# Kernel optimization log

Hardware: AMD Instinct MI355X
Metric: run time of the kernel (lower is better)

Reference implementation:

```python
import jax, jax.numpy as jnp
import numpy as np

TOP_K = 9  # ATSSMatcher default


def setup_inputs() -> dict:
    key = jax.random.key(0)
    k1, k2, k3, k4 = jax.random.split(key, 4)
    N, M = 120000, 800
    IMG = 1024.0
    # anchors: valid x1<x2, y1<y2 boxes
    a_ctr = jax.random.uniform(k1, (N, 2)) * IMG
    a_sz = jax.random.uniform(k2, (N, 2)) * 60.0 + 8.0
    anchors = jnp.concatenate([a_ctr - a_sz / 2, a_ctr + a_sz / 2], axis=1)
    g_ctr = jax.random.uniform(k3, (M, 2)) * IMG
    g_sz = jax.random.uniform(k4, (M, 2)) * 100.0 + 10.0
    gt_boxes = jnp.concatenate([g_ctr - g_sz / 2, g_ctr + g_sz / 2], axis=1)
    return {"anchors": anchors, "gt_boxes": gt_boxes}


def _box_iou(a, b):
    # a: [N,4], b: [M,4] -> [N,M]
    area_a = (a[:, 2] - a[:, 0]) * (a[:, 3] - a[:, 1])
    area_b = (b[:, 2] - b[:, 0]) * (b[:, 3] - b[:, 1])
    lt = jnp.maximum(a[:, None, :2], b[None, :, :2])
    rb = jnp.minimum(a[:, None, 2:], b[None, :, 2:])
    wh = jnp.clip(rb - lt, 0.0)
    inter = wh[..., 0] * wh[..., 1]
    union = area_a[:, None] + area_b[None, :] - inter
    return inter / jnp.maximum(union, 1e-12)


def reference(anchors, gt_boxes):
    N = anchors.shape[0]
    M = gt_boxes.shape[0]
    ious = _box_iou(anchors, gt_boxes)                         # [N, M]
    a_ctr = (anchors[:, :2] + anchors[:, 2:]) / 2              # [N, 2]
    g_ctr = (gt_boxes[:, :2] + gt_boxes[:, 2:]) / 2            # [M, 2]
    # center distances [M, N] (per-GT rows for top-k along last axis)
    d = jnp.linalg.norm(a_ctr[None, :, :] - g_ctr[:, None, :], axis=-1)
    _, topk_idx = jax.lax.top_k(-d, TOP_K)                     # [M, TOP_K] nearest anchors
    topk_ious = jnp.take_along_axis(ious.T, topk_idx, axis=1)  # [M, TOP_K]
    iou_mean = topk_ious.mean(axis=1)                          # [M]
    iou_std = jnp.std(topk_ious, axis=1, ddof=1)               # torch .std() is unbiased
    thresh = iou_mean + iou_std                                # [M]
    candidate = ious >= thresh[None, :]                        # [N, M]
    cx, cy = a_ctr[:, 0], a_ctr[:, 1]
    inside = ((cx[:, None] >= gt_boxes[None, :, 0]) &
              (cx[:, None] <= gt_boxes[None, :, 2]) &
              (cy[:, None] >= gt_boxes[None, :, 1]) &
              (cy[:, None] <= gt_boxes[None, :, 3]))           # [N, M]
    pos = candidate & inside                                   # [N, M]
    gt_ids = jnp.arange(M, dtype=jnp.int32)[None, :]
    matched_idxs = jnp.max(jnp.where(pos, gt_ids, -1), axis=1)  # [N]
    gathered = jnp.take_along_axis(
        ious, jnp.clip(matched_idxs, 0)[:, None].astype(jnp.int32), axis=1)[:, 0]
    max_ious = jnp.where(matched_idxs >= 0, gathered, 0.0)
    return matched_idxs.astype(jnp.int64), max_ious
```

## Files before the change

kernel.cpp:

```cpp
#include <hip/hip_runtime.h>
#include <stdint.h>

typedef unsigned int u32;
typedef unsigned long long u64;

#define TOPK 9
#define GA 64
#define CELL_A 16.0f
#define NCA (GA * GA)
#define GG 16
#define CELL_G 64.0f
#define NCG (GG * GG)
#define CAPA 96
#define CAPG 160
#define OVA 8192
#define OVG 1024

__global__ __launch_bounds__(256) void zero_counts(u32* __restrict__ p, int n)
{
    int i = blockIdx.x * 256 + threadIdx.x;
    if (i < n) p[i] = 0u;
}

__global__ __launch_bounds__(256) void bucket_insert(
    const float4* __restrict__ a4, const float4* __restrict__ g4,
    u32* __restrict__ cursA, u32* __restrict__ cursG, u32* __restrict__ ovfCnt,
    float4* __restrict__ slotA, float4* __restrict__ gtBox,
    u32* __restrict__ gtBkt,
    u32* __restrict__ ovAidx, float2* __restrict__ ovActr,
    u32* __restrict__ ovGidx, int N, int M)
{
    int gid = blockIdx.x * 256 + threadIdx.x;
    if (gid < N) {
        float4 a = a4[gid];
        float cx = (a.x + a.z) * 0.5f;
        float cy = (a.y + a.w) * 0.5f;
        int ix = min(GA - 1, max(0, (int)(cx * (1.0f / CELL_A))));
        int iy = min(GA - 1, max(0, (int)(cy * (1.0f / CELL_A))));
        int cell = iy * GA + ix;
        u32 p = atomicAdd(&cursA[cell], 1u);
        if (p < CAPA) {
            slotA[cell * CAPA + p] =
                make_float4(cx, cy, __uint_as_float((u32)gid), 0.f);
        } else {
            u32 q = atomicAdd(&ovfCnt[0], 1u);
            if (q < OVA) { ovAidx[q] = (u32)gid; ovActr[q] = make_float2(cx, cy); }
        }
    } else if (gid < N + M) {
        int m = gid - N;
        float4 g = g4[m];
        int ix0 = min(GG - 1, max(0, (int)floorf(g.x * (1.0f / CELL_G))));
        int iy0 = min(GG - 1, max(0, (int)floorf(g.y * (1.0f / CELL_G))));
        int ix1 = min(GG - 1, max(0, (int)floorf(g.z * (1.0f / CELL_G))));
        int iy1 = min(GG - 1, max(0, (int)floorf(g.w * (1.0f / CELL_G))));
        for (int j = iy0; j <= iy1; ++j)
            for (int i = ix0; i <= ix1; ++i) {
                int cell = j * GG + i;
                u32 p = atomicAdd(&cursG[cell], 1u);
                if (p < CAPG) {
                    gtBox[cell * CAPG + p] = g;
                    gtBkt[cell * CAPG + p] = (u32)m;
                } else {
                    u32 q = atomicAdd(&ovfCnt[1], 1u);
                    if (q < OVG) ovGidx[q] = (u32)m;
                }
            }
    }
}

__global__ __launch_bounds__(256) void atss_query(
    const float4* __restrict__ a4, const float* __restrict__ gts,
    const u32* __restrict__ cursA, const float4* __restrict__ slotA,
    const u32* __restrict__ ovfCnt,
    const u32* __restrict__ ovAidx, const float2* __restrict__ ovActr,
    float* __restrict__ thresh, int M)
{
    const int m = blockIdx.x;
    if (m >= M) return;
    const int tid  = (int)threadIdx.x;
    const int wid  = tid >> 6;
    const int lane = tid & 63;

    __shared__ u32   s_cnt[4];
    __shared__ float s_max[4];
    __shared__ u64   s_top[4 * TOPK];

    const float gx0 = gts[m * 4 + 0], gy0 = gts[m * 4 + 1];
    const float gx1 = gts[m * 4 + 2], gy1 = gts[m * 4 + 3];
    const float gcx = (gx0 + gx1) * 0.5f;
    const float gcy = (gy0 + gy1) * 0.5f;
    const int ci = min(GA - 1, max(0, (int)(gcx * (1.0f / CELL_A))));
    const int cj = min(GA - 1, max(0, (int)(gcy * (1.0f / CELL_A))));

    {
        const int r = wid;
        const int ncell = (r == 0) ? 1 : 8 * r;
        u32 myc = 0;
        float mymax = 0.f;
        for (int k = lane; k < ncell; k += 64) {
            int di = 0, dj = 0;
            if (r > 0) {
                int side = k / (2 * r), pos = k % (2 * r);
                if (side == 0)      { di = -r + pos; dj = -r; }
                else if (side == 1) { di = r;        dj = -r + pos; }
                else if (side == 2) { di = r - pos;  dj = r; }
                else                { di = -r;       dj = r - pos; }
            }
            int i = ci + di, j = cj + dj;
            if (i < 0 || i >= GA || j < 0 || j >= GA) continue;
            u32 cnt = cursA[j * GA + i];
            if (cnt) {
                myc += cnt;
                float x0 = i * CELL_A, x1 = x0 + CELL_A;
                float y0 = j * CELL_A, y1 = y0 + CELL_A;
                float dxm = fmaxf(gcx - x0, x1 - gcx);
                float dym = fmaxf(gcy - y0, y1 - gcy);
                mymax = fmaxf(mymax, dxm * dxm + dym * dym);
            }
        }
#pragma unroll
        for (int s2 = 1; s2 <= 32; s2 <<= 1) {
            myc += __shfl_xor(myc, s2, 64);
            mymax = fmaxf(mymax, __shfl_xor(mymax, s2, 64));
        }
        if (lane == 0) { s_cnt[wid] = myc; s_max[wid] = mymax; }
    }
    __syncthreads();

    u32 cum = 0;
    float maxd2 = 0.f;
#pragma unroll
    for (int r = 0; r < 4; ++r) {
        if (cum < TOPK) {
            cum += s_cnt[r];
            maxd2 = fmaxf(maxd2, s_max[r]);
        }
    }
    if (cum < TOPK) {
        for (int r = 4; r < GA && cum < TOPK; ++r) {
            const int ncell = 8 * r;
            u32 myc = 0;
            float mymax = 0.f;
            for (int k = lane; k < ncell; k += 64) {
                int side = k / (2 * r), pos = k % (2 * r);
                int di, dj;
                if (side == 0)      { di = -r + pos; dj = -r; }
                else if (side == 1) { di = r;        dj = -r + pos; }
                else if (side == 2) { di = r - pos;  dj = r; }
                else                { di = -r;       dj = r - pos; }
                int i = ci + di, j = cj + dj;
                if (i < 0 || i >= GA || j < 0 || j >= GA) continue;
                u32 cnt = cursA[j * GA + i];
                if (cnt) {
                    myc += cnt;
                    float x0 = i * CELL_A, x1 = x0 + CELL_A;
                    float y0 = j * CELL_A, y1 = y0 + CELL_A;
                    float dxm = fmaxf(gcx - x0, x1 - gcx);
                    float dym = fmaxf(gcy - y0, y1 - gcy);
                    mymax = fmaxf(mymax, dxm * dxm + dym * dym);
                }
            }
#pragma unroll
            for (int s2 = 1; s2 <= 32; s2 <<= 1) {
                myc += __shfl_xor(myc, s2, 64);
                mymax = fmaxf(mymax, __shfl_xor(mymax, s2, 64));
            }
            cum += myc;
            maxd2 = fmaxf(maxd2, mymax);
        }
    }
    const float D2pad = maxd2 * 1.0001f + 1.0f;

    u64 kk[TOPK];
#pragma unroll
    for (int i = 0; i < TOPK; ++i) kk[i] = ~0ULL;

    const int rs = 1 + (int)(sqrtf(D2pad) * (1.0f / CELL_A));
    const int jlo = max(0, cj - rs), jhi = min(GA - 1, cj + rs);
    const int ilo = max(0, ci - rs), ihi = min(GA - 1, ci + rs);
    const int ncols  = ihi - ilo + 1;
    const int ncells = (jhi - jlo + 1) * ncols;
    for (int t = wid; t < ncells; t += 4) {
        int j = jlo + t / ncols;
        int i = ilo + t % ncols;
        float y0 = j * CELL_A, y1 = y0 + CELL_A;
        float mdy = fmaxf(fmaxf(y0 - gcy, gcy - y1), 0.f);
        float x0 = i * CELL_A, x1 = x0 + CELL_A;
        float mdx = fmaxf(fmaxf(x0 - gcx, gcx - x1), 0.f);
        if (mdx * mdx + mdy * mdy > D2pad) continue;
        int c = j * GA + i;
        u32 cnt = min(cursA[c], (u32)CAPA);
        u32 base = (u32)c * CAPA;
        for (u32 tc = lane; tc < cnt; tc += 64) {
            float4 s = slotA[base + tc];
            float ddx = s.x - gcx, ddy = s.y - gcy;
            float d2 = ddx * ddx + ddy * ddy;
            if (d2 <= D2pad) {
                float d = sqrtf(d2);
                u64 key = ((u64)__float_as_uint(d) << 32) | __float_as_uint(s.z);
                if (key < kk[TOPK - 1]) {
                    u64 t2 = key;
#pragma unroll
                    for (int q = 0; q < TOPK; ++q) {
                        u64 lo = (kk[q] < t2) ? kk[q] : t2;
                        u64 hi = (kk[q] < t2) ? t2 : kk[q];
                        kk[q] = lo;
                        t2 = hi;
                    }
                }
            }
        }
    }
    {
        u32 nov = min(ovfCnt[0], (u32)OVA);
        for (u32 tc = (u32)tid; tc < nov; tc += 256) {
            u32 n = ovAidx[tc];
            float2 cc = ovActr[tc];
            float ddx = cc.x - gcx, ddy = cc.y - gcy;
            float d2 = ddx * ddx + ddy * ddy;
            if (d2 <= D2pad) {
                float d = sqrtf(d2);
                u64 key = ((u64)__float_as_uint(d) << 32) | n;
                if (key < kk[TOPK - 1]) {
                    u64 t2 = key;
#pragma unroll
                    for (int q = 0; q < TOPK; ++q) {
                        u64 lo = (kk[q] < t2) ? kk[q] : t2;
                        u64 hi = (kk[q] < t2) ? t2 : kk[q];
                        kk[q] = lo;
                        t2 = hi;
                    }
                }
            }
        }
    }

    {
        u64 wv;
#pragma unroll
        for (int rd = 0; rd < TOPK; ++rd) {
            wv = kk[0];
#pragma unroll
            for (int s2 = 1; s2 <= 32; s2 <<= 1) {
                u64 o = __shfl_xor(wv, s2, 64);
                if (o < wv) wv = o;
            }
            if (lane == 0) s_top[wid * TOPK + rd] = wv;
            if (kk[0] == wv) {
#pragma unroll
                for (int q = 0; q < TOPK - 1; ++q) kk[q] = kk[q + 1];
                kk[TOPK - 1] = ~0ULL;
            }
        }
    }
    __syncthreads();

    if (wid == 0) {
        u64 v = (lane < 4 * TOPK) ? s_top[lane] : ~0ULL;
        u64 wins[TOPK];
#pragma unroll
        for (int rd = 0; rd < TOPK; ++rd) {
            u64 wv = v;
#pragma unroll
            for (int s2 = 1; s2 <= 32; s2 <<= 1) {
                u64 o = __shfl_xor(wv, s2, 64);
                if (o < wv) wv = o;
            }
            wins[rd] = wv;
            if (v == wv) v = ~0ULL;
        }

        if (lane == 0) {
            const float area_g = (gx1 - gx0) * (gy1 - gy0);
            float vals[TOPK];
            float sum = 0.f;
#pragma unroll
            for (int r = 0; r < TOPK; ++r) {
                int idx = (int)(u32)(wins[r] & 0xffffffffULL);
                float4 a = a4[idx];
                float area_a = (a.z - a.x) * (a.w - a.y);
                float ltx = fmaxf(a.x, gx0), lty = fmaxf(a.y, gy0);
                float rbx = fminf(a.z, gx1), rby = fminf(a.w, gy1);
                float w2 = fmaxf(rbx - ltx, 0.f);
                float h2 = fmaxf(rby - lty, 0.f);
                float inter = w2 * h2;
                float uni = area_a + area_g - inter;
                float iou = inter / fmaxf(uni, 1e-12f);
                vals[r] = iou;
                sum += iou;
            }
            float mean = sum / 9.0f;
            float var = 0.f;
#pragma unroll
            for (int r = 0; r < TOPK; ++r) {
                float d2 = vals[r] - mean;
                var += d2 * d2;
            }
            float sd = sqrtf(var / 8.0f);
            thresh[m] = mean + sd;
        }
    }
}

__global__ __launch_bounds__(256) void atss_assign(
    const float4* __restrict__ a4, const float4* __restrict__ g4,
    const float* __restrict__ thresh,
    const u32* __restrict__ cursG, const float4* __restrict__ gtBox,
    const u32* __restrict__ gtBkt,
    const u32* __restrict__ ovfCnt, const u32* __restrict__ ovGidx,
    float* __restrict__ out_idx, float* __restrict__ out_iou, int N, int M)
{
    int n = blockIdx.x * 256 + threadIdx.x;
    if (n >= N) return;

    float4 a = a4[n];
    float area_a = (a.z - a.x) * (a.w - a.y);
    float cx = (a.x + a.z) * 0.5f;
    float cy = (a.y + a.w) * 0.5f;

    int ig = min(GG - 1, max(0, (int)(cx * (1.0f / CELL_G))));
    int jg = min(GG - 1, max(0, (int)(cy * (1.0f / CELL_G))));
    int cell = jg * GG + ig;

    u64 best = 0;
    u32 cnt = min(cursG[cell], (u32)CAPG);
    u32 base = (u32)cell * CAPG;
    for (u32 t2 = 0; t2 < cnt; ++t2) {
        float4 g = gtBox[base + t2];
        if (cx >= g.x && cx <= g.z && cy >= g.y && cy <= g.w) {
            int mi = (int)gtBkt[base + t2];
            float area_g = (g.z - g.x) * (g.w - g.y);
            float ltx = fmaxf(a.x, g.x), lty = fmaxf(a.y, g.y);
            float rbx = fminf(a.z, g.z), rby = fminf(a.w, g.w);
            float w = fmaxf(rbx - ltx, 0.f);
            float h = fmaxf(rby - lty, 0.f);
            float inter = w * h;
            float uni = area_a + area_g - inter;
            float iou = inter / fmaxf(uni, 1e-12f);
            if (iou >= thresh[mi]) {
                u64 cand = ((u64)(u32)(mi + 1) << 32) | __float_as_uint(iou);
                if (cand > best) best = cand;
            }
        }
    }
    {
        u32 nog = min(ovfCnt[1], (u32)OVG);
        for (u32 t2 = 0; t2 < nog; ++t2) {
            int mi = (int)ovGidx[t2];
            float4 g = g4[mi];
            if (cx >= g.x && cx <= g.z && cy >= g.y && cy <= g.w) {
                float area_g = (g.z - g.x) * (g.w - g.y);
                float ltx = fmaxf(a.x, g.x), lty = fmaxf(a.y, g.y);
                float rbx = fminf(a.z, g.z), rby = fminf(a.w, g.w);
                float w = fmaxf(rbx - ltx, 0.f);
                float h = fmaxf(rby - lty, 0.f);
                float inter = w * h;
                float uni = area_a + area_g - inter;
                float iou = inter / fmaxf(uni, 1e-12f);
                if (iou >= thresh[mi]) {
                    u64 cand = ((u64)(u32)(mi + 1) << 32) | __float_as_uint(iou);
                    if (cand > best) best = cand;
                }
            }
        }
    }

    int mm = (int)(best >> 32) - 1;
    out_idx[n] = (float)mm;
    out_iou[n] = (mm >= 0) ? __uint_as_float((u32)best) : 0.f;
}

__global__ __launch_bounds__(256) void fb_centers(
    const float4* __restrict__ a4, float2* __restrict__ c2, int N)
{
    int n = blockIdx.x * 256 + threadIdx.x;
    if (n < N) {
        float4 a = a4[n];
        c2[n] = make_float2((a.x + a.z) * 0.5f, (a.y + a.w) * 0.5f);
    }
}

__global__ __launch_bounds__(256) void fb_thresh(
    const float4* __restrict__ a4, const float2* __restrict__ c2,
    const float* __restrict__ gts, float* __restrict__ thresh, int N)
{
    const int m = blockIdx.x;
    const int tid = threadIdx.x;
    const float gx0 = gts[m * 4 + 0], gy0 = gts[m * 4 + 1];
    const float gx1 = gts[m * 4 + 2], gy1 = gts[m * 4 + 3];
    const float gcx = (gx0 + gx1) * 0.5f;
    const float gcy = (gy0 + gy1) * 0.5f;

    float vmin = __builtin_inff();
    for (int n = tid; n < N; n += 512) {
        float2 c = c2[n];
        float dx = c.x - gcx, dy = c.y - gcy;
        vmin = fminf(vmin, dx * dx + dy * dy);
    }
    float v = vmin, w = 0.f;
#pragma unroll
    for (int r = 0; r < TOPK; ++r) {
        float t = v;
#pragma unroll
        for (int s = 1; s <= 32; s <<= 1) t = fminf(t, __shfl_xor(t, s, 64));
        w = t;
        if (v == w) v = __builtin_inff();
    }
    const float T = sqrtf(w) * 1.0001f + 1e-6f;

    u64 k[TOPK];
#pragma unroll
    for (int i = 0; i < TOPK; ++i) k[i] = ~0ULL;
    for (int n = tid; n < N; n += 256) {
        float2 c = c2[n];
        float dx = c.x - gcx, dy = c.y - gcy;
        float d = sqrtf(dx * dx + dy * dy);
        if (d <= T) {
            u64 key = ((u64)__float_as_uint(d) << 32) | (unsigned)n;
            if (key < k[TOPK - 1]) {
                u64 t = key;
#pragma unroll
                for (int i = 0; i < TOPK; ++i) {
                    u64 lo = (k[i] < t) ? k[i] : t;
                    u64 hi = (k[i] < t) ? t : k[i];
                    k[i] = lo;
                    t = hi;
                }
            }
        }
    }
    __shared__ u64 red[256];
    __shared__ int top9[TOPK];
#pragma unroll 1
    for (int r = 0; r < TOPK; ++r) {
        red[tid] = k[0];
        __syncthreads();
        for (int s = 128; s > 0; s >>= 1) {
            if (tid < s) {
                u64 o = red[tid + s];
                if (o < red[tid]) red[tid] = o;
            }
            __syncthreads();
        }
        u64 win = red[0];
        if (tid == 0) top9[r] = (int)(unsigned)(win & 0xffffffffULL);
        __syncthreads();
        if (k[0] == win) {
#pragma unroll
            for (int i = 0; i < TOPK - 1; ++i) k[i] = k[i + 1];
            k[TOPK - 1] = ~0ULL;
        }
    }
    if (tid == 0) {
        const float area_g = (gx1 - gx0) * (gy1 - gy0);
        float vals[TOPK];
        float s = 0.f;
#pragma unroll
        for (int r = 0; r < TOPK; ++r) {
            float4 a = a4[top9[r]];
            float area_a = (a.z - a.x) * (a.w - a.y);
            float ltx = fmaxf(a.x, gx0), lty = fmaxf(a.y, gy0);
            float rbx = fminf(a.z, gx1), rby = fminf(a.w, gy1);
            float w2 = fmaxf(rbx - ltx, 0.f);
            float h2 = fmaxf(rby - lty, 0.f);
            float inter = w2 * h2;
            float uni = area_a + area_g - inter;
            float iou = inter / fmaxf(uni, 1e-12f);
            vals[r] = iou;
            s += iou;
        }
        float mean = s / 9.0f;
        float var = 0.f;
#pragma unroll
        for (int r = 0; r < TOPK; ++r) {
            float d2 = vals[r] - mean;
            var += d2 * d2;
        }
        thresh[m] = mean + sqrtf(var / 8.0f);
    }
}

__global__ __launch_bounds__(256) void fb_assign(
    const float4* __restrict__ a4, const float4* __restrict__ g4,
    const float* __restrict__ thresh,
    float* __restrict__ out_idx, float* __restrict__ out_iou, int N, int M)
{
    extern __shared__ char smem[];
    float4* sg = (float4*)smem;
    float2* se = (float2*)(smem + (size_t)M * 16);
    for (int i = threadIdx.x; i < M; i += 256) {
        float4 g = g4[i];
        sg[i] = g;
        se[i] = make_float2((g.z - g.x) * (g.w - g.y), thresh[i]);
    }
    __syncthreads();
    int n = blockIdx.x * 256 + threadIdx.x;
    if (n >= N) return;
    float4 a = a4[n];
    float area_a = (a.z - a.x) * (a.w - a.y);
    float cx = (a.x + a.z) * 0.5f;
    float cy = (a.y + a.w) * 0.5f;
    u64 best = 0;
    for (int mi = 0; mi < M; ++mi) {
        float4 g = sg[mi];
        if (cx >= g.x && cx <= g.z && cy >= g.y && cy <= g.w) {
            float2 e = se[mi];
            float ltx = fmaxf(a.x, g.x), lty = fmaxf(a.y, g.y);
            float rbx = fminf(a.z, g.z), rby = fminf(a.w, g.w);
            float w = fmaxf(rbx - ltx, 0.f);
            float h = fmaxf(rby - lty, 0.f);
            float inter = w * h;
            float uni = area_a + e.x - inter;
            float iou = inter / fmaxf(uni, 1e-12f);
            if (iou >= e.y)
                best = ((u64)(u32)(mi + 1) << 32) | __float_as_uint(iou);
        }
    }
    int mm = (int)(best >> 32) - 1;
    out_idx[n] = (float)mm;
    out_iou[n] = (mm >= 0) ? __uint_as_float((u32)best) : 0.f;
}

extern "C" void kernel_launch(void* const* d_in, const int* in_sizes, int n_in,
                              void* d_out, int out_size, void* d_ws, size_t ws_size,
                              hipStream_t stream) {
    const float4* a4 = (const float4*)d_in[0];
    const float4* g4 = (const float4*)d_in[1];
    const float* gts = (const float*)d_in[1];
    const int N = in_sizes[0] / 4;
    const int M = in_sizes[1] / 4;

    const size_t oCursA  = 0;
    const size_t oCursG  = oCursA + NCA;
    const size_t oOvfCnt = oCursG + NCG;
    const size_t oThresh = oOvfCnt + 2;
    size_t oSlotA = oThresh + (size_t)M;
    oSlotA = (oSlotA + 3) & ~(size_t)3;
    const size_t oGtBox  = oSlotA + 4 * (size_t)NCA * CAPA;
    const size_t oGtBkt  = oGtBox + 4 * (size_t)NCG * CAPG;
    const size_t oOvAidx = oGtBkt + (size_t)NCG * CAPG;
    size_t oOvActr = oOvAidx + OVA;
    oOvActr = (oOvActr + 1) & ~(size_t)1;
    const size_t oOvGidx = oOvActr + 2 * (size_t)OVA;
    const size_t needBytes = (oOvGidx + OVG) * sizeof(u32);

    if (ws_size >= needBytes) {
        u32* w = (u32*)d_ws;
        u32* cursA    = w + oCursA;
        u32* cursG    = w + oCursG;
        u32* ovfCnt   = w + oOvfCnt;
        float* thr    = (float*)(w + oThresh);
        float4* slotA = (float4*)(w + oSlotA);
        float4* gtBox = (float4*)(w + oGtBox);
        u32* gtBkt    = w + oGtBkt;
        u32* ovAidx   = w + oOvAidx;
        float2* ovActr= (float2*)(w + oOvActr);
        u32* ovGidx   = w + oOvGidx;

        const int nZero = NCA + NCG + 2;
        zero_counts<<<(nZero + 255) / 256, 256, 0, stream>>>(cursA, nZero);
        bucket_insert<<<(N + M + 255) / 256, 256, 0, stream>>>(
            a4, g4, cursA, cursG, ovfCnt, slotA, gtBox, gtBkt,
            ovAidx, ovActr, ovGidx, N, M);
        atss_query<<<M, 256, 0, stream>>>(
            a4, gts, cursA, slotA, ovfCnt, ovAidx, ovActr, thr, M);
        atss_assign<<<(N + 255) / 256, 256, 0, stream>>>(
            a4, g4, thr, cursG, gtBox, gtBkt, ovfCnt, ovGidx,
            (float*)d_out, (float*)d_out + N, N, M);
    } else {
        float* thr = (float*)d_ws;
        float2* centers = (float2*)d_out;
        fb_centers<<<(N + 255) / 256, 256, 0, stream>>>(a4, centers, N);
        fb_thresh<<<M, 256, 0, stream>>>(a4, (const float2*)centers, gts, thr, N);
        size_t lds = (size_t)M * 24;
        fb_assign<<<(N + 255) / 256, 256, lds, stream>>>(
            a4, g4, thr, (float*)d_out, (float*)d_out + N, N, M);
    }
}
```

Before: 49.71 us.

## Fuse four launches into two cooperative kernels with in-kernel grid synchronisation

```diff
diff --git a/kernel.cpp b/kernel.cpp
--- a/kernel.cpp
+++ b/kernel.cpp
@@ -15,6 +15,446 @@
 #define CAPG 160
 #define OVA 8192
 #define OVG 1024
+
+#define MAGA 0x5A17C3D9u
+#define MAGB 0xA6E83C26u
+
+__device__ __forceinline__ u32 aload(const u32* p) {
+    return __hip_atomic_load(p, __ATOMIC_RELAXED, __HIP_MEMORY_SCOPE_AGENT);
+}
+__device__ __forceinline__ void astore(u32* p, u32 v) {
+    __hip_atomic_store(p, v, __ATOMIC_RELAXED, __HIP_MEMORY_SCOPE_AGENT);
+}
+
+#define ZN (NCA + NCG + 2 + 1)
+
+__global__ __launch_bounds__(256) void insert_init(
+    const float4* __restrict__ a4, const float4* __restrict__ g4,
+    u32* __restrict__ w, int N, int M)
+{
+    const size_t oCursA  = 0;
+    const size_t oCursG  = oCursA + NCA;
+    const size_t oOvfCnt = oCursG + NCG;
+    const size_t oQdone  = oOvfCnt + 2;
+    const size_t oMag    = oQdone + 1;
+    size_t oThresh = oMag + 2;
+    size_t oSlotA  = (oThresh + (size_t)M + 3) & ~(size_t)3;
+    const size_t oGtBox  = oSlotA + 4 * (size_t)NCA * CAPA;
+    const size_t oGtBkt  = oGtBox + 4 * (size_t)NCG * CAPG;
+    const size_t oOvAidx = oGtBkt + (size_t)NCG * CAPG;
+    size_t oOvActr = (oOvAidx + OVA + 1) & ~(size_t)1;
+    const size_t oOvGidx = oOvActr + 2 * (size_t)OVA;
+
+    u32* cursA    = w + oCursA;
+    u32* cursG    = w + oCursG;
+    u32* ovfCnt   = w + oOvfCnt;
+    u32* mag      = w + oMag;
+    float4* slotA = (float4*)(w + oSlotA);
+    float4* gtBox = (float4*)(w + oGtBox);
+    u32* gtBkt    = w + oGtBkt;
+    u32* ovAidx   = w + oOvAidx;
+    float2* ovActr= (float2*)(w + oOvActr);
+    u32* ovGidx   = w + oOvGidx;
+
+    const int tid = (int)threadIdx.x;
+    const int bid = (int)blockIdx.x;
+
+    if (bid == 0) {
+        for (int i = tid; i < ZN; i += 256) astore(&w[i], 0u);
+        asm volatile("s_waitcnt vmcnt(0)" ::: "memory");
+        __syncthreads();
+        if (tid == 0) { astore(&mag[0], MAGA); astore(&mag[1], MAGB); }
+    } else {
+        if (tid == 0) {
+            while (!(aload(&mag[0]) == MAGA && aload(&mag[1]) == MAGB))
+                __builtin_amdgcn_s_sleep(4);
+        }
+        __syncthreads();
+    }
+
+    const int gstride = (int)gridDim.x * 256;
+    for (int gid = bid * 256 + tid; gid < N + M; gid += gstride) {
+        if (gid < N) {
+            float4 a = a4[gid];
+            float cx = (a.x + a.z) * 0.5f;
+            float cy = (a.y + a.w) * 0.5f;
+            int ix = min(GA - 1, max(0, (int)(cx * (1.0f / CELL_A))));
+            int iy = min(GA - 1, max(0, (int)(cy * (1.0f / CELL_A))));
+            int cell = iy * GA + ix;
+            u32 p = atomicAdd(&cursA[cell], 1u);
+            if (p < CAPA) {
+                slotA[cell * CAPA + p] =
+                    make_float4(cx, cy, __uint_as_float((u32)gid), 0.f);
+            } else {
+                u32 q = atomicAdd(&ovfCnt[0], 1u);
+                if (q < OVA) { ovAidx[q] = (u32)gid; ovActr[q] = make_float2(cx, cy); }
+            }
+        } else {
+            int m = gid - N;
+            float4 g = g4[m];
+            int ix0 = min(GG - 1, max(0, (int)floorf(g.x * (1.0f / CELL_G))));
+            int iy0 = min(GG - 1, max(0, (int)floorf(g.y * (1.0f / CELL_G))));
+            int ix1 = min(GG - 1, max(0, (int)floorf(g.z * (1.0f / CELL_G))));
+            int iy1 = min(GG - 1, max(0, (int)floorf(g.w * (1.0f / CELL_G))));
+            for (int j = iy0; j <= iy1; ++j)
+                for (int i = ix0; i <= ix1; ++i) {
+                    int cell = j * GG + i;
+                    u32 p = atomicAdd(&cursG[cell], 1u);
+                    if (p < CAPG) {
+                        gtBox[cell * CAPG + p] = g;
+                        gtBkt[cell * CAPG + p] = (u32)m;
+                    } else {
+                        u32 q = atomicAdd(&ovfCnt[1], 1u);
+                        if (q < OVG) ovGidx[q] = (u32)m;
+                    }
+                }
+        }
+    }
+}
+
+__global__ __launch_bounds__(256) void qa_fused(
+    const float4* __restrict__ a4, const float4* __restrict__ g4,
+    u32* __restrict__ w, float* __restrict__ outp, int N, int M)
+{
+    const size_t oCursA  = 0;
+    const size_t oCursG  = oCursA + NCA;
+    const size_t oOvfCnt = oCursG + NCG;
+    const size_t oQdone  = oOvfCnt + 2;
+    const size_t oMag    = oQdone + 1;
+    size_t oThresh = oMag + 2;
+    size_t oSlotA  = (oThresh + (size_t)M + 3) & ~(size_t)3;
+    const size_t oGtBox  = oSlotA + 4 * (size_t)NCA * CAPA;
+    const size_t oGtBkt  = oGtBox + 4 * (size_t)NCG * CAPG;
+    const size_t oOvAidx = oGtBkt + (size_t)NCG * CAPG;
+    size_t oOvActr = (oOvAidx + OVA + 1) & ~(size_t)1;
+    const size_t oOvGidx = oOvActr + 2 * (size_t)OVA;
+
+    const u32* cursA    = w + oCursA;
+    const u32* cursG    = w + oCursG;
+    const u32* ovfCnt   = w + oOvfCnt;
+    u32* qdone          = w + oQdone;
+    u32* mag            = w + oMag;
+    u32* thr            = w + oThresh;
+    const float4* slotA = (const float4*)(w + oSlotA);
+    const float4* gtBox = (const float4*)(w + oGtBox);
+    const u32* gtBkt    = w + oGtBkt;
+    const u32* ovAidx   = w + oOvAidx;
+    const float2* ovActr= (const float2*)(w + oOvActr);
+    const u32* ovGidx   = w + oOvGidx;
+    const float* gts = (const float*)g4;
+    float* out_idx = outp;
+    float* out_iou = outp + N;
+
+    const int tid  = (int)threadIdx.x;
+    const int bid  = (int)blockIdx.x;
+    const int nblk = (int)gridDim.x;
+    const int wid  = tid >> 6;
+    const int lane = tid & 63;
+
+    __shared__ u32   s_cnt[4];
+    __shared__ float s_max[4];
+    __shared__ u64   s_top[4 * TOPK];
+    __shared__ float s_thr[2048];
+
+    for (int m = bid; m < M; m += nblk) {
+        const float gx0 = gts[m * 4 + 0], gy0 = gts[m * 4 + 1];
+        const float gx1 = gts[m * 4 + 2], gy1 = gts[m * 4 + 3];
+        const float gcx = (gx0 + gx1) * 0.5f;
+        const float gcy = (gy0 + gy1) * 0.5f;
+        const int ci = min(GA - 1, max(0, (int)(gcx * (1.0f / CELL_A))));
+        const int cj = min(GA - 1, max(0, (int)(gcy * (1.0f / CELL_A))));
+
+        {
+            const int r = wid;
+            const int ncell = (r == 0) ? 1 : 8 * r;
+            u32 myc = 0;
+            float mymax = 0.f;
+            for (int k = lane; k < ncell; k += 64) {
+                int di = 0, dj = 0;
+                if (r > 0) {
+                    int side = k / (2 * r), pos = k % (2 * r);
+                    if (side == 0)      { di = -r + pos; dj = -r; }
+                    else if (side == 1) { di = r;        dj = -r + pos; }
+                    else if (side == 2) { di = r - pos;  dj = r; }
+                    else                { di = -r;       dj = r - pos; }
+                }
+                int i = ci + di, j = cj + dj;
+                if (i < 0 || i >= GA || j < 0 || j >= GA) continue;
+                u32 cnt = cursA[j * GA + i];
+                if (cnt) {
+                    myc += cnt;
+                    float x0 = i * CELL_A, x1 = x0 + CELL_A;
+                    float y0 = j * CELL_A, y1 = y0 + CELL_A;
+                    float dxm = fmaxf(gcx - x0, x1 - gcx);
+                    float dym = fmaxf(gcy - y0, y1 - gcy);
+                    mymax = fmaxf(mymax, dxm * dxm + dym * dym);
+                }
+            }
+#pragma unroll
+            for (int s2 = 1; s2 <= 32; s2 <<= 1) {
+                myc += __shfl_xor(myc, s2, 64);
+                mymax = fmaxf(mymax, __shfl_xor(mymax, s2, 64));
+            }
+            if (lane == 0) { s_cnt[wid] = myc; s_max[wid] = mymax; }
+        }
+        __syncthreads();
+
+        u32 cum = 0;
+        float maxd2 = 0.f;
+#pragma unroll
+        for (int r = 0; r < 4; ++r) {
+            if (cum < TOPK) {
+                cum += s_cnt[r];
+                maxd2 = fmaxf(maxd2, s_max[r]);
+            }
+        }
+        __syncthreads();
+        if (cum < TOPK) {
+            for (int r = 4; r < GA && cum < TOPK; ++r) {
+                const int ncell = 8 * r;
+                u32 myc = 0;
+                float mymax = 0.f;
+                for (int k = lane; k < ncell; k += 64) {
+                    int side = k / (2 * r), pos = k % (2 * r);
+                    int di, dj;
+                    if (side == 0)      { di = -r + pos; dj = -r; }
+                    else if (side == 1) { di = r;        dj = -r + pos; }
+                    else if (side == 2) { di = r - pos;  dj = r; }
+                    else                { di = -r;       dj = r - pos; }
+                    int i = ci + di, j = cj + dj;
+                    if (i < 0 || i >= GA || j < 0 || j >= GA) continue;
+                    u32 cnt = cursA[j * GA + i];
+                    if (cnt) {
+                        myc += cnt;
+                        float x0 = i * CELL_A, x1 = x0 + CELL_A;
+                        float y0 = j * CELL_A, y1 = y0 + CELL_A;
+                        float dxm = fmaxf(gcx - x0, x1 - gcx);
+                        float dym = fmaxf(gcy - y0, y1 - gcy);
+                        mymax = fmaxf(mymax, dxm * dxm + dym * dym);
+                    }
+                }
+#pragma unroll
+                for (int s2 = 1; s2 <= 32; s2 <<= 1) {
+                    myc += __shfl_xor(myc, s2, 64);
+                    mymax = fmaxf(mymax, __shfl_xor(mymax, s2, 64));
+                }
+                cum += myc;
+                maxd2 = fmaxf(maxd2, mymax);
+            }
+        }
+        const float D2pad = maxd2 * 1.0001f + 1.0f;
+
+        u64 kk[TOPK];
+#pragma unroll
+        for (int i = 0; i < TOPK; ++i) kk[i] = ~0ULL;
+
+        const int rs = 1 + (int)(sqrtf(D2pad) * (1.0f / CELL_A));
+        const int jlo = max(0, cj - rs), jhi = min(GA - 1, cj + rs);
+        const int ilo = max(0, ci - rs), ihi = min(GA - 1, ci + rs);
+        const int ncols  = ihi - ilo + 1;
+        const int ncells = (jhi - jlo + 1) * ncols;
+        for (int t = wid; t < ncells; t += 4) {
+            int j = jlo + t / ncols;
+            int i = ilo + t % ncols;
+            float y0 = j * CELL_A, y1 = y0 + CELL_A;
+            float mdy = fmaxf(fmaxf(y0 - gcy, gcy - y1), 0.f);
+            float x0 = i * CELL_A, x1 = x0 + CELL_A;
+            float mdx = fmaxf(fmaxf(x0 - gcx, gcx - x1), 0.f);
+            if (mdx * mdx + mdy * mdy > D2pad) continue;
+            int c = j * GA + i;
+            u32 cnt = min(cursA[c], (u32)CAPA);
+            u32 base = (u32)c * CAPA;
+            for (u32 tc = lane; tc < cnt; tc += 64) {
+                float4 s = slotA[base + tc];
+                float ddx = s.x - gcx, ddy = s.y - gcy;
+                float d2 = ddx * ddx + ddy * ddy;
+                if (d2 <= D2pad) {
+                    float d = sqrtf(d2);
+                    u64 key = ((u64)__float_as_uint(d) << 32) | __float_as_uint(s.z);
+                    if (key < kk[TOPK - 1]) {
+                        u64 t2 = key;
+#pragma unroll
+                        for (int q = 0; q < TOPK; ++q) {
+                            u64 lo = (kk[q] < t2) ? kk[q] : t2;
+                            u64 hi = (kk[q] < t2) ? t2 : kk[q];
+                            kk[q] = lo;
+                            t2 = hi;
+                        }
+                    }
+                }
+            }
+        }
+        {
+            u32 nov = min(ovfCnt[0], (u32)OVA);
+            for (u32 tc = (u32)tid; tc < nov; tc += 256) {
+                u32 n = ovAidx[tc];
+                float2 cc = ovActr[tc];
+                float ddx = cc.x - gcx, ddy = cc.y - gcy;
+                float d2 = ddx * ddx + ddy * ddy;
+                if (d2 <= D2pad) {
+                    float d = sqrtf(d2);
+                    u64 key = ((u64)__float_as_uint(d) << 32) | n;
+                    if (key < kk[TOPK - 1]) {
+                        u64 t2 = key;
+#pragma unroll
+                        for (int q = 0; q < TOPK; ++q) {
+                            u64 lo = (kk[q] < t2) ? kk[q] : t2;
+                            u64 hi = (kk[q] < t2) ? t2 : kk[q];
+                            kk[q] = lo;
+                            t2 = hi;
+                        }
+                    }
+                }
+            }
+        }
+
+        {
+#pragma unroll
+            for (int rd = 0; rd < TOPK; ++rd) {
+                u64 wv = kk[0];
+#pragma unroll
+                for (int s2 = 1; s2 <= 32; s2 <<= 1) {
+                    u64 o = __shfl_xor(wv, s2, 64);
+                    if (o < wv) wv = o;
+                }
+                if (lane == 0) s_top[wid * TOPK + rd] = wv;
+                if (kk[0] == wv) {
+#pragma unroll
+                    for (int q = 0; q < TOPK - 1; ++q) kk[q] = kk[q + 1];
+                    kk[TOPK - 1] = ~0ULL;
+                }
+            }
+        }
+        __syncthreads();
+
+        if (wid == 0) {
+            u64 v = (lane < 4 * TOPK) ? s_top[lane] : ~0ULL;
+            u64 wins[TOPK];
+#pragma unroll
+            for (int rd = 0; rd < TOPK; ++rd) {
+                u64 wv = v;
+#pragma unroll
+                for (int s2 = 1; s2 <= 32; s2 <<= 1) {
+                    u64 o = __shfl_xor(wv, s2, 64);
+                    if (o < wv) wv = o;
+                }
+                wins[rd] = wv;
+                if (v == wv) v = ~0ULL;
+            }
+
+            if (lane == 0) {
+                const float area_g = (gx1 - gx0) * (gy1 - gy0);
+                float vals[TOPK];
+                float sum = 0.f;
+#pragma unroll
+                for (int r = 0; r < TOPK; ++r) {
+                    int idx = (int)(u32)(wins[r] & 0xffffffffULL);
+                    float4 a = a4[idx];
+                    float area_a = (a.z - a.x) * (a.w - a.y);
+                    float ltx = fmaxf(a.x, gx0), lty = fmaxf(a.y, gy0);
+                    float rbx = fminf(a.z, gx1), rby = fminf(a.w, gy1);
+                    float w2 = fmaxf(rbx - ltx, 0.f);
+                    float h2 = fmaxf(rby - lty, 0.f);
+                    float inter = w2 * h2;
+                    float uni = area_a + area_g - inter;
+                    float iou = inter / fmaxf(uni, 1e-12f);
+                    vals[r] = iou;
+                    sum += iou;
+                }
+                float mean = sum / 9.0f;
+                float var = 0.f;
+#pragma unroll
+                for (int r = 0; r < TOPK; ++r) {
+                    float d2 = vals[r] - mean;
+                    var += d2 * d2;
+                }
+                float sd = sqrtf(var / 8.0f);
+                astore(&thr[m], __float_as_uint(mean + sd));
+                asm volatile("s_waitcnt vmcnt(0)" ::: "memory");
+                __hip_atomic_fetch_add(qdone, 1u, __ATOMIC_RELAXED,
+                                       __HIP_MEMORY_SCOPE_AGENT);
+            }
+        }
+        __syncthreads();
+    }
+
+    if (tid == 0) {
+        while (aload(qdone) < (u32)M) __builtin_amdgcn_s_sleep(4);
+    }
+    __syncthreads();
+    if (bid == 0 && tid == 0) {
+        astore(&mag[0], 0u);
+        astore(&mag[1], 0u);
+    }
+
+    const bool useLds = (M <= 2048);
+    if (useLds) {
+        for (int i = tid; i < M; i += 256)
+            s_thr[i] = __uint_as_float(aload(&thr[i]));
+        __syncthreads();
+    }
+
+    const int gstride = nblk * 256;
+    for (int n = bid * 256 + tid; n < N; n += gstride) {
+        float4 a = a4[n];
+        float area_a = (a.z - a.x) * (a.w - a.y);
+        float cx = (a.x + a.z) * 0.5f;
+        float cy = (a.y + a.w) * 0.5f;
+
+        int ig = min(GG - 1, max(0, (int)(cx * (1.0f / CELL_G))));
+        int jg = min(GG - 1, max(0, (int)(cy * (1.0f / CELL_G))));
+        int cell = jg * GG + ig;
+
+        u64 best = 0;
+        u32 cnt = min(cursG[cell], (u32)CAPG);
+        u32 base = (u32)cell * CAPG;
+        for (u32 t2 = 0; t2 < cnt; ++t2) {
+            float4 g = gtBox[base + t2];
+            if (cx >= g.x && cx <= g.z && cy >= g.y && cy <= g.w) {
+                int mi = (int)gtBkt[base + t2];
+                float area_g = (g.z - g.x) * (g.w - g.y);
+                float ltx = fmaxf(a.x, g.x), lty = fmaxf(a.y, g.y);
+                float rbx = fminf(a.z, g.z), rby = fminf(a.w, g.w);
+                float ww = fmaxf(rbx - ltx, 0.f);
+                float hh = fmaxf(rby - lty, 0.f);
+                float inter = ww * hh;
+                float uni = area_a + area_g - inter;
+                float iou = inter / fmaxf(uni, 1e-12f);
+                float tv = useLds ? s_thr[mi] : __uint_as_float(aload(&thr[mi]));
+                if (iou >= tv) {
+                    u64 cand = ((u64)(u32)(mi + 1) << 32) | __float_as_uint(iou);
+                    if (cand > best) best = cand;
+                }
+            }
+        }
+        {
+            u32 nog = min(ovfCnt[1], (u32)OVG);
+            for (u32 t2 = 0; t2 < nog; ++t2) {
+                int mi = (int)ovGidx[t2];
+                float4 g = g4[mi];
+                if (cx >= g.x && cx <= g.z && cy >= g.y && cy <= g.w) {
+                    float area_g = (g.z - g.x) * (g.w - g.y);
+                    float ltx = fmaxf(a.x, g.x), lty = fmaxf(a.y, g.y);
+                    float rbx = fminf(a.z, g.z), rby = fminf(a.w, g.w);
+                    float ww = fmaxf(rbx - ltx, 0.f);
+                    float hh = fmaxf(rby - lty, 0.f);
+                    float inter = ww * hh;
+                    float uni = area_a + area_g - inter;
+                    float iou = inter / fmaxf(uni, 1e-12f);
+                    float tv = useLds ? s_thr[mi] : __uint_as_float(aload(&thr[mi]));
+                    if (iou >= tv) {
+                        u64 cand = ((u64)(u32)(mi + 1) << 32) | __float_as_uint(iou);
+                        if (cand > best) best = cand;
+                    }
+                }
+            }
+        }
+
+        int mm = (int)(best >> 32) - 1;
+        out_idx[n] = (float)mm;
+        out_iou[n] = (mm >= 0) ? __uint_as_float((u32)best) : 0.f;
+    }
+}
 
 __global__ __launch_bounds__(256) void zero_counts(u32* __restrict__ p, int n)
 {
@@ -236,10 +676,9 @@
     }
 
     {
-        u64 wv;
 #pragma unroll
         for (int rd = 0; rd < TOPK; ++rd) {
-            wv = kk[0];
+            u64 wv = kk[0];
 #pragma unroll
             for (int s2 = 1; s2 <= 32; s2 <<= 1) {
                 u64 o = __shfl_xor(wv, s2, 64);
@@ -527,47 +966,87 @@
     const float4* a4 = (const float4*)d_in[0];
     const float4* g4 = (const float4*)d_in[1];
     const float* gts = (const float*)d_in[1];
-    const int N = in_sizes[0] / 4;
-    const int M = in_sizes[1] / 4;
+    int N = in_sizes[0] / 4;
+    int M = in_sizes[1] / 4;
 
     const size_t oCursA  = 0;
     const size_t oCursG  = oCursA + NCA;
     const size_t oOvfCnt = oCursG + NCG;
-    const size_t oThresh = oOvfCnt + 2;
-    size_t oSlotA = oThresh + (size_t)M;
-    oSlotA = (oSlotA + 3) & ~(size_t)3;
+    const size_t oQdone  = oOvfCnt + 2;
+    const size_t oMag    = oQdone + 1;
+    size_t oThresh = oMag + 2;
+    size_t oSlotA  = (oThresh + (size_t)M + 3) & ~(size_t)3;
     const size_t oGtBox  = oSlotA + 4 * (size_t)NCA * CAPA;
     const size_t oGtBkt  = oGtBox + 4 * (size_t)NCG * CAPG;
     const size_t oOvAidx = oGtBkt + (size_t)NCG * CAPG;
-    size_t oOvActr = oOvAidx + OVA;
-    oOvActr = (oOvActr + 1) & ~(size_t)1;
+    size_t oOvActr = (oOvAidx + OVA + 1) & ~(size_t)1;
     const size_t oOvGidx = oOvActr + 2 * (size_t)OVA;
     const size_t needBytes = (oOvGidx + OVG) * sizeof(u32);
 
+    bool done = false;
     if (ws_size >= needBytes) {
         u32* w = (u32*)d_ws;
-        u32* cursA    = w + oCursA;
-        u32* cursG    = w + oCursG;
-        u32* ovfCnt   = w + oOvfCnt;
-        float* thr    = (float*)(w + oThresh);
-        float4* slotA = (float4*)(w + oSlotA);
-        float4* gtBox = (float4*)(w + oGtBox);
-        u32* gtBkt    = w + oGtBkt;
-        u32* ovAidx   = w + oOvAidx;
-        float2* ovActr= (float2*)(w + oOvActr);
-        u32* ovGidx   = w + oOvGidx;
-
-        const int nZero = NCA + NCG + 2;
-        zero_counts<<<(nZero + 255) / 256, 256, 0, stream>>>(cursA, nZero);
-        bucket_insert<<<(N + M + 255) / 256, 256, 0, stream>>>(
-            a4, g4, cursA, cursG, ovfCnt, slotA, gtBox, gtBkt,
-            ovAidx, ovActr, ovGidx, N, M);
-        atss_query<<<M, 256, 0, stream>>>(
-            a4, gts, cursA, slotA, ovfCnt, ovAidx, ovActr, thr, M);
-        atss_assign<<<(N + 255) / 256, 256, 0, stream>>>(
-            a4, g4, thr, cursG, gtBox, gtBkt, ovfCnt, ovGidx,
-            (float*)d_out, (float*)d_out + N, N, M);
-    } else {
+        float* outf = (float*)d_out;
+
+        static int cap1 = -2, cap2 = -2;
+        if (cap1 == -2) {
+            int mb1 = 0, mb2 = 0, ncu = 0, dev = 0;
+            if (hipOccupancyMaxActiveBlocksPerMultiprocessor(
+                    &mb1, (const void*)insert_init, 256, 0) != hipSuccess) mb1 = 0;
+            if (hipOccupancyMaxActiveBlocksPerMultiprocessor(
+                    &mb2, (const void*)qa_fused, 256, 0) != hipSuccess) mb2 = 0;
+            hipGetDevice(&dev);
+            if (hipDeviceGetAttribute(&ncu, hipDeviceAttributeMultiprocessorCount,
+                                      dev) != hipSuccess) ncu = 0;
+            cap1 = mb1 * ncu;
+            cap2 = mb2 * ncu;
+        }
+
+        if (cap1 >= 64 && cap2 >= 64) {
+            int need1 = (N + M + 255) / 256;
+            int need2 = (N + 255) / 256;
+            if (M > need2) need2 = M;
+            int nb1 = need1 < cap1 ? need1 : cap1;
+            int nb2 = need2 < cap2 ? need2 : cap2;
+            void* a1[] = { (void*)&a4, (void*)&g4, (void*)&w, (void*)&N, (void*)&M };
+            hipError_t e1 = hipLaunchCooperativeKernel((const void*)insert_init,
+                                                       dim3((unsigned)nb1), dim3(256),
+                                                       a1, 0, stream);
+            if (e1 == hipSuccess) {
+                void* a2[] = { (void*)&a4, (void*)&g4, (void*)&w, (void*)&outf,
+                               (void*)&N, (void*)&M };
+                hipError_t e2 = hipLaunchCooperativeKernel((const void*)qa_fused,
+                                                           dim3((unsigned)nb2), dim3(256),
+                                                           a2, 0, stream);
+                done = (e2 == hipSuccess);
+            }
+        }
+
+        if (!done) {
+            u32* cursA    = w + oCursA;
+            u32* cursG    = w + oCursG;
+            u32* ovfCnt   = w + oOvfCnt;
+            float* thr    = (float*)(w + oThresh);
+            float4* slotA = (float4*)(w + oSlotA);
+            float4* gtBox = (float4*)(w + oGtBox);
+            u32* gtBkt    = w + oGtBkt;
+            u32* ovAidx   = w + oOvAidx;
+            float2* ovActr= (float2*)(w + oOvActr);
+            u32* ovGidx   = w + oOvGidx;
+
+            zero_counts<<<(ZN + 255) / 256, 256, 0, stream>>>(cursA, ZN);
+            bucket_insert<<<(N + M + 255) / 256, 256, 0, stream>>>(
+                a4, g4, cursA, cursG, ovfCnt, slotA, gtBox, gtBkt,
+                ovAidx, ovActr, ovGidx, N, M);
+            atss_query<<<M, 256, 0, stream>>>(
+                a4, gts, cursA, slotA, ovfCnt, ovAidx, ovActr, thr, M);
+            atss_assign<<<(N + 255) / 256, 256, 0, stream>>>(
+                a4, g4, thr, cursG, gtBox, gtBkt, ovfCnt, ovGidx,
+                (float*)d_out, (float*)d_out + N, N, M);
+            done = true;
+        }
+    }
+    if (!done) {
         float* thr = (float*)d_ws;
         float2* centers = (float2*)d_out;
         fb_centers<<<(N + 255) / 256, 256, 0, stream>>>(a4, centers, N);
```

After: 115.5 us. 2.32x slower.
